# Optimization experiments

Hardware: AMD Instinct MI355X
Metric: run time of the kernel (lower is better)

Reference implementation:

```python
import jax, jax.numpy as jnp
import numpy as np

N = 100000   # nodes
E = 1000000  # edges
F_IN = 128
H = 256
G = 64       # graphs in batch
EPS = 1e-5   # BatchNorm eps


def setup_inputs() -> dict:
    key = jax.random.key(0)
    ks = jax.random.split(key, 16)
    s = 0.05
    d = {}
    d["x"] = jax.random.normal(ks[0], (N, F_IN), jnp.float32)
    d["edge_index"] = jax.random.randint(ks[1], (2, E), 0, N, dtype=jnp.int32)
    d["batch"] = jnp.sort(jax.random.randint(ks[2], (N,), 0, G, dtype=jnp.int32))
    # block1 (128 -> 256, has projection)
    d["W1"] = jax.random.normal(ks[3], (F_IN, H), jnp.float32) * s
    d["b1"] = jnp.zeros((H,), jnp.float32)
    d["g1"] = jnp.ones((H,), jnp.float32)
    d["be1"] = jnp.zeros((H,), jnp.float32)
    d["P1"] = jax.random.normal(ks[4], (F_IN, H), jnp.float32) * s
    # blocks 2-4 (256 -> 256)
    for i, k in zip((2, 3, 4), (ks[5], ks[6], ks[7])):
        d[f"W{i}"] = jax.random.normal(k, (H, H), jnp.float32) * s
        d[f"b{i}"] = jnp.zeros((H,), jnp.float32)
        d[f"g{i}"] = jnp.ones((H,), jnp.float32)
        d[f"be{i}"] = jnp.zeros((H,), jnp.float32)
    d["Wl"] = jax.random.normal(ks[8], (H, 1), jnp.float32) * s
    d["bl"] = jnp.zeros((1,), jnp.float32)
    return d


def _gcn_norm(edge_index):
    # PyG gcn_norm: add self-loops, deg from dst column, norm = d^-1/2[src]*d^-1/2[dst]
    src, dst = edge_index[0], edge_index[1]
    deg = jax.ops.segment_sum(jnp.ones((E,), jnp.float32), dst, num_segments=N) + 1.0
    dis = jax.lax.rsqrt(deg)
    enorm = dis[src] * dis[dst]          # [E] normalization per edge
    self_w = 1.0 / deg                   # self-loop weight = deg^-1
    return src, dst, enorm, self_w


def _block(x, src, dst, enorm, self_w, W, b, g, be, P=None):
    hw = x @ W                                            # [N, H]
    msg = hw[src] * enorm[:, None]                        # [E, H] gather
    agg = jax.ops.segment_sum(msg, dst, num_segments=N)   # scatter-add
    agg = agg + hw * self_w[:, None] + b                  # self-loop + bias
    # BatchNorm1d (training-mode batch statistics, biased variance)
    m = jnp.mean(agg, axis=0)
    v = jnp.var(agg, axis=0)
    out = jax.nn.relu((agg - m) * jax.lax.rsqrt(v + EPS) * g + be)
    res = x @ P if P is not None else x
    return out + res


def reference(x, edge_index, batch, W1, b1, g1, be1, P1,
              W2, b2, g2, be2, W3, b3, g3, be3, W4, b4, g4, be4, Wl, bl):
    src, dst, enorm, self_w = _gcn_norm(edge_index)
    h = _block(x, src, dst, enorm, self_w, W1, b1, g1, be1, P1)
    h = _block(h, src, dst, enorm, self_w, W2, b2, g2, be2)
    h = _block(h, src, dst, enorm, self_w, W3, b3, g3, be3)
    h = _block(h, src, dst, enorm, self_w, W4, b4, g4, be4)
    # global mean pool over graphs
    sums = jax.ops.segment_sum(h, batch, num_segments=G)                       # [G, H]
    cnt = jax.ops.segment_sum(jnp.ones((N,), jnp.float32), batch, num_segments=G)
    pooled = sums / jnp.maximum(cnt, 1.0)[:, None]
    return pooled @ Wl + bl                                                    # [G, 1]
```

## Files before the change

### kernel.cpp

```cpp
#include <hip/hip_runtime.h>
#include <cstdint>
#include <cstddef>

#define NN 100000
#define NE 1000000
#define FIN 128
#define HD 256
#define NG 64
#define BNEPS 1e-5f

typedef unsigned short ushort_t;
typedef __attribute__((ext_vector_type(8))) short bf16x8;
typedef __attribute__((ext_vector_type(4))) float f32x4;


__device__ inline float b2f(unsigned short u) {
    union { float f; unsigned int i; } x; x.i = ((unsigned int)u) << 16; return x.f;
}
__device__ inline unsigned short f2b(float f) {
    union { float f; unsigned int i; } x; x.f = f;
    unsigned int r = x.i + 0x7FFFu + ((x.i >> 16) & 1u);
    return (unsigned short)(r >> 16);
}
__device__ inline float  ld1(const unsigned short* p) { return b2f(*p); }
__device__ inline float4 ld4v(const unsigned short* p) {
    ushort4 u = *(const ushort4*)p;
    return make_float4(b2f(u.x), b2f(u.y), b2f(u.z), b2f(u.w));
}
__device__ inline float2 ld2v(const unsigned short* p) {
    ushort2 u = *(const ushort2*)p;
    return make_float2(b2f(u.x), b2f(u.y));
}
__device__ inline void st4v(unsigned short* p, float4 v) {
    ushort4 u; u.x = f2b(v.x); u.y = f2b(v.y); u.z = f2b(v.z); u.w = f2b(v.w);
    *(ushort4*)p = u;
}
__device__ inline void st2v(unsigned short* p, float2 v) {
    ushort2 u; u.x = f2b(v.x); u.y = f2b(v.y);
    *(ushort2*)p = u;
}


__global__ __launch_bounds__(256) void count_deg_k(const int* __restrict__ dst, int* __restrict__ cnt) {
    int e = blockIdx.x * 256 + threadIdx.x;
    if (e < NE) atomicAdd(&cnt[dst[e]], 1);
}

__global__ __launch_bounds__(256) void node_prep_k(const int* __restrict__ cnt,
                                                   float* __restrict__ dis, float* __restrict__ selfw) {
    int i = blockIdx.x * 256 + threadIdx.x;
    if (i < NN) {
        float d = (float)cnt[i] + 1.0f;
        dis[i] = rsqrtf(d);
        selfw[i] = 1.0f / d;
    }
}

__global__ __launch_bounds__(1024) void scan_reduce_k(const int* __restrict__ cnt, int* __restrict__ partials) {
    __shared__ int sh[1024];
    int i = blockIdx.x * 1024 + threadIdx.x;
    sh[threadIdx.x] = (i < NN) ? cnt[i] : 0;
    __syncthreads();
    for (int off = 512; off > 0; off >>= 1) {
        if (threadIdx.x < off) sh[threadIdx.x] += sh[threadIdx.x + off];
        __syncthreads();
    }
    if (threadIdx.x == 0) partials[blockIdx.x] = sh[0];
}

__global__ void scan_partials_k(int* partials, int nb) {
    if (threadIdx.x == 0 && blockIdx.x == 0) {
        int run = 0;
        for (int b = 0; b < nb; b++) { int v = partials[b]; partials[b] = run; run += v; }
    }
}

__global__ __launch_bounds__(1024) void scan_write_k(const int* __restrict__ cnt,
                                                     const int* __restrict__ partials,
                                                     int* __restrict__ rowptr) {
    __shared__ int sh[1024];
    int i = blockIdx.x * 1024 + threadIdx.x;
    int v = (i < NN) ? cnt[i] : 0;
    sh[threadIdx.x] = v;
    __syncthreads();
    for (int off = 1; off < 1024; off <<= 1) {
        int t = (threadIdx.x >= off) ? sh[threadIdx.x - off] : 0;
        __syncthreads();
        sh[threadIdx.x] += t;
        __syncthreads();
    }
    if (i < NN) rowptr[i] = partials[blockIdx.x] + sh[threadIdx.x] - v;
    if (i == NN - 1) rowptr[NN] = partials[blockIdx.x] + sh[threadIdx.x];
}

__global__ __launch_bounds__(256) void fill_csr_k(const int* __restrict__ src, const int* __restrict__ dst,
                                                  const int* __restrict__ rowptr, int* __restrict__ cursor,
                                                  const float* __restrict__ dis,
                                                  int2* __restrict__ csr) {
    int e = blockIdx.x * 256 + threadIdx.x;
    if (e < NE) {
        int d = dst[e], s = src[e];
        int pos = rowptr[d] + atomicAdd(&cursor[d], 1);
        float w = dis[s] * dis[d];
        csr[pos] = make_int2(s, __float_as_int(w));
    }
}

__global__ __launch_bounds__(256) void x2b_k(const float* __restrict__ x, unsigned short* __restrict__ xb) {
    int i = blockIdx.x * 256 + threadIdx.x;
    if (i < NN * FIN / 4) {
        float4 v = *reinterpret_cast<const float4*>(x + (size_t)i * 4);
        ushort4 u; u.x = f2b(v.x); u.y = f2b(v.y); u.z = f2b(v.z); u.w = f2b(v.w);
        *reinterpret_cast<ushort4*>(xb + (size_t)i * 4) = u;
    }
}

__global__ __launch_bounds__(256) void wt_all_k(const float* __restrict__ W1, const float* __restrict__ P1,
                                                const float* __restrict__ W2, const float* __restrict__ W3,
                                                const float* __restrict__ W4,
                                                unsigned short* __restrict__ w1t, unsigned short* __restrict__ p1t,
                                                unsigned short* __restrict__ w2t, unsigned short* __restrict__ w3t,
                                                unsigned short* __restrict__ w4t) {
    int b = blockIdx.x;
    const float* W; unsigned short* Bt; int K; int base;
    if (b < 128)      { W = W1; Bt = w1t; K = 128; base = b; }
    else if (b < 256) { W = P1; Bt = p1t; K = 128; base = b - 128; }
    else if (b < 512) { W = W2; Bt = w2t; K = 256; base = b - 256; }
    else if (b < 768) { W = W3; Bt = w3t; K = 256; base = b - 512; }
    else              { W = W4; Bt = w4t; K = 256; base = b - 768; }
    int i = base * 256 + threadIdx.x;
    if (i < K * 256) {
        int k = i >> 8, n = i & 255;
        Bt[n * K + k] = f2b(W[k * 256 + n]);
    }
}


template<int COLS>
__global__ __launch_bounds__(256) void spmm_k(const unsigned short* __restrict__ h,
                                              const int* __restrict__ rowptr,
                                              const int2* __restrict__ csr,
                                              const float* __restrict__ selfw,
                                              unsigned short* __restrict__ z) {
    const int lane = threadIdx.x & 63;
    const int row = blockIdx.x * 4 + (threadIdx.x >> 6);
    if (row >= NN) return;
    if constexpr (COLS == 256) {
        float4 a = ld4v(h + (size_t)row * COLS + lane * 4);
        float sw = selfw[row];
        float4 acc = make_float4(a.x * sw, a.y * sw, a.z * sw, a.w * sw);
        int e = rowptr[row];
        const int e1 = rowptr[row + 1];
        for (; e + 8 <= e1; e += 8) {
            int2 cc[8];
#pragma unroll
            for (int j = 0; j < 8; j++) cc[j] = csr[e + j];
            float4 hv[8];
#pragma unroll
            for (int j = 0; j < 8; j++) hv[j] = ld4v(h + (size_t)cc[j].x * COLS + lane * 4);
#pragma unroll
            for (int j = 0; j < 8; j++) {
                float w = __int_as_float(cc[j].y);
                acc.x += w * hv[j].x; acc.y += w * hv[j].y; acc.z += w * hv[j].z; acc.w += w * hv[j].w;
            }
        }
        for (; e + 4 <= e1; e += 4) {
            int2 c0 = csr[e], c1 = csr[e + 1], c2 = csr[e + 2], c3 = csr[e + 3];
            float4 h0 = ld4v(h + (size_t)c0.x * COLS + lane * 4);
            float4 h1 = ld4v(h + (size_t)c1.x * COLS + lane * 4);
            float4 h2 = ld4v(h + (size_t)c2.x * COLS + lane * 4);
            float4 h3 = ld4v(h + (size_t)c3.x * COLS + lane * 4);
            float w0 = __int_as_float(c0.y), w1 = __int_as_float(c1.y);
            float w2 = __int_as_float(c2.y), w3 = __int_as_float(c3.y);
            acc.x += w0 * h0.x; acc.y += w0 * h0.y; acc.z += w0 * h0.z; acc.w += w0 * h0.w;
            acc.x += w1 * h1.x; acc.y += w1 * h1.y; acc.z += w1 * h1.z; acc.w += w1 * h1.w;
            acc.x += w2 * h2.x; acc.y += w2 * h2.y; acc.z += w2 * h2.z; acc.w += w2 * h2.w;
            acc.x += w3 * h3.x; acc.y += w3 * h3.y; acc.z += w3 * h3.z; acc.w += w3 * h3.w;
        }
        for (; e < e1; e++) {
            int2 c = csr[e];
            float w = __int_as_float(c.y);
            float4 hv = ld4v(h + (size_t)c.x * COLS + lane * 4);
            acc.x += w * hv.x; acc.y += w * hv.y; acc.z += w * hv.z; acc.w += w * hv.w;
        }
        st4v(z + (size_t)row * COLS + lane * 4, acc);
    } else {
        float2 a = ld2v(h + (size_t)row * COLS + lane * 2);
        float sw = selfw[row];
        float2 acc = make_float2(a.x * sw, a.y * sw);
        int e = rowptr[row];
        const int e1 = rowptr[row + 1];
        for (; e + 8 <= e1; e += 8) {
            int2 cc[8];
#pragma unroll
            for (int j = 0; j < 8; j++) cc[j] = csr[e + j];
            float2 hv[8];
#pragma unroll
            for (int j = 0; j < 8; j++) hv[j] = ld2v(h + (size_t)cc[j].x * COLS + lane * 2);
#pragma unroll
            for (int j = 0; j < 8; j++) {
                float w = __int_as_float(cc[j].y);
                acc.x += w * hv[j].x; acc.y += w * hv[j].y;
            }
        }
        for (; e + 4 <= e1; e += 4) {
            int2 c0 = csr[e], c1 = csr[e + 1], c2 = csr[e + 2], c3 = csr[e + 3];
            float2 h0 = ld2v(h + (size_t)c0.x * COLS + lane * 2);
            float2 h1 = ld2v(h + (size_t)c1.x * COLS + lane * 2);
            float2 h2 = ld2v(h + (size_t)c2.x * COLS + lane * 2);
            float2 h3 = ld2v(h + (size_t)c3.x * COLS + lane * 2);
            float w0 = __int_as_float(c0.y), w1 = __int_as_float(c1.y);
            float w2 = __int_as_float(c2.y), w3 = __int_as_float(c3.y);
            acc.x += w0 * h0.x; acc.y += w0 * h0.y;
            acc.x += w1 * h1.x; acc.y += w1 * h1.y;
            acc.x += w2 * h2.x; acc.y += w2 * h2.y;
            acc.x += w3 * h3.x; acc.y += w3 * h3.y;
        }
        for (; e < e1; e++) {
            int2 c = csr[e];
            float w = __int_as_float(c.y);
            float2 hv = ld2v(h + (size_t)c.x * COLS + lane * 2);
            acc.x += w * hv.x; acc.y += w * hv.y;
        }
        st2v(z + (size_t)row * COLS + lane * 2, acc);
    }
}


#define RPB 391

template<int K, int MODE>
__global__ __launch_bounds__(512, 4) void mgemm_k(const unsigned short* __restrict__ A,
                                                  const unsigned short* __restrict__ Bt,
                                                  const float* __restrict__ bias,
                                                  unsigned short* __restrict__ C,
                                                  const float* __restrict__ scale,
                                                  const float* __restrict__ shift,
                                                  const unsigned short* __restrict__ aggin,
                                                  float* __restrict__ sums, int M) {
    constexpr int NCOLS = 128;
    constexpr int NF = NCOLS / 16;
    constexpr int SEGS = K / 8;
    constexpr int KS = K / 32;
    __shared__ char Bl[NCOLS * K * 2];
    __shared__ float sstat[2 * NCOLS];
    const int tid  = threadIdx.x;
    const int lane = tid & 63;
    const int wid  = tid >> 6;
    const int q    = lane >> 4;
    const int rl   = lane & 15;
    const int col0 = blockIdx.y * NCOLS;
    const int rbase = blockIdx.x * RPB;
    const int rend  = min(rbase + RPB, M);

    for (int s = tid; s < NCOLS * SEGS; s += 512) {
        int col = s / SEGS, j = s % SEGS;
        uint4 v = *reinterpret_cast<const uint4*>(Bt + (size_t)(col0 + col) * K + j * 8);
        *reinterpret_cast<uint4*>(Bl + col * (K * 2) + (((j) ^ (col & 7)) << 4)) = v;
    }
    if (MODE == 0 && tid < 2 * NCOLS) sstat[tid] = 0.f;
    __syncthreads();

    for (int it = 0; it < 2; it++) {
        const int row0 = rbase + it * 256 + wid * 32;
        if (row0 >= rend) continue;

        const int a0r = min(row0 + rl, M - 1);
        const int a1r = min(row0 + 16 + rl, M - 1);
        const unsigned short* pa0 = A + (size_t)a0r * K + q * 8;
        const unsigned short* pa1 = A + (size_t)a1r * K + q * 8;

        f32x4 acc[2][NF];
#pragma unroll
        for (int m = 0; m < 2; m++)
#pragma unroll
            for (int n = 0; n < NF; n++) acc[m][n] = (f32x4){0.f, 0.f, 0.f, 0.f};

#pragma unroll
        for (int ks = 0; ks < KS; ks++) {
            bf16x8 af0 = *reinterpret_cast<const bf16x8*>(pa0 + ks * 32);
            bf16x8 af1 = *reinterpret_cast<const bf16x8*>(pa1 + ks * 32);
#pragma unroll
            for (int nf = 0; nf < NF; nf++) {
                int col = nf * 16 + rl;
                bf16x8 bf = *reinterpret_cast<const bf16x8*>(Bl + col * (K * 2) + (((ks * 4 + q) ^ (col & 7)) << 4));
                acc[0][nf] = __builtin_amdgcn_mfma_f32_16x16x32_bf16(bf, af0, acc[0][nf], 0, 0, 0);
                acc[1][nf] = __builtin_amdgcn_mfma_f32_16x16x32_bf16(bf, af1, acc[1][nf], 0, 0, 0);
            }
        }

        const int g0 = row0 + rl, g1 = row0 + 16 + rl;
        const bool ok0 = g0 < rend, ok1 = g1 < rend;
#pragma unroll
        for (int nf = 0; nf < NF; nf++) {
            int cb = col0 + nf * 16 + q * 4;
            f32x4 v0 = acc[0][nf], v1 = acc[1][nf];
            if (MODE == 0) {
                float4 bb = *reinterpret_cast<const float4*>(bias + cb);
                v0[0] += bb.x; v0[1] += bb.y; v0[2] += bb.z; v0[3] += bb.w;
                v1[0] += bb.x; v1[1] += bb.y; v1[2] += bb.z; v1[3] += bb.w;
            } else {
                float4 sc = *reinterpret_cast<const float4*>(scale + cb);
                float4 sh = *reinterpret_cast<const float4*>(shift + cb);
                if (ok0) {
                    ushort4 ag = *reinterpret_cast<const ushort4*>(aggin + (size_t)g0 * HD + cb);
                    v0[0] += fmaxf(fmaf(b2f(ag.x), sc.x, sh.x), 0.f);
                    v0[1] += fmaxf(fmaf(b2f(ag.y), sc.y, sh.y), 0.f);
                    v0[2] += fmaxf(fmaf(b2f(ag.z), sc.z, sh.z), 0.f);
                    v0[3] += fmaxf(fmaf(b2f(ag.w), sc.w, sh.w), 0.f);
                }
                if (ok1) {
                    ushort4 ag = *reinterpret_cast<const ushort4*>(aggin + (size_t)g1 * HD + cb);
                    v1[0] += fmaxf(fmaf(b2f(ag.x), sc.x, sh.x), 0.f);
                    v1[1] += fmaxf(fmaf(b2f(ag.y), sc.y, sh.y), 0.f);
                    v1[2] += fmaxf(fmaf(b2f(ag.z), sc.z, sh.z), 0.f);
                    v1[3] += fmaxf(fmaf(b2f(ag.w), sc.w, sh.w), 0.f);
                }
            }
            if (ok0) {
                ushort4 u; u.x = f2b(v0[0]); u.y = f2b(v0[1]); u.z = f2b(v0[2]); u.w = f2b(v0[3]);
                *reinterpret_cast<ushort4*>(C + (size_t)g0 * HD + cb) = u;
            }
            if (ok1) {
                ushort4 u; u.x = f2b(v1[0]); u.y = f2b(v1[1]); u.z = f2b(v1[2]); u.w = f2b(v1[3]);
                *reinterpret_cast<ushort4*>(C + (size_t)g1 * HD + cb) = u;
            }
            if (MODE == 0) {
                if (!ok0) { v0[0] = v0[1] = v0[2] = v0[3] = 0.f; }
                if (!ok1) { v1[0] = v1[1] = v1[2] = v1[3] = 0.f; }
                float s[4], qq[4];
#pragma unroll
                for (int j = 0; j < 4; j++) {
                    s[j]  = v0[j] + v1[j];
                    qq[j] = v0[j] * v0[j] + v1[j] * v1[j];
                }
#pragma unroll
                for (int m = 1; m < 16; m <<= 1) {
#pragma unroll
                    for (int j = 0; j < 4; j++) {
                        s[j]  += __shfl_xor(s[j], m, 64);
                        qq[j] += __shfl_xor(qq[j], m, 64);
                    }
                }
                if (rl == 0) {
                    int cl = nf * 16 + q * 4;
#pragma unroll
                    for (int j = 0; j < 4; j++) {
                        atomicAdd(&sstat[cl + j], s[j]);
                        atomicAdd(&sstat[NCOLS + cl + j], qq[j]);
                    }
                }
            }
        }
    }

    if (MODE == 0) {
        __syncthreads();
        if (tid < NCOLS)            atomicAdd(&sums[col0 + tid], sstat[tid]);
        else if (tid < 2 * NCOLS)   atomicAdd(&sums[HD + col0 + (tid - NCOLS)], sstat[tid]);
    }
}


__global__ void bn_fin_k(const float* __restrict__ sums, const float* __restrict__ g,
                         const float* __restrict__ be, float* __restrict__ sc, float* __restrict__ sh) {
    int c = threadIdx.x;
    float m = sums[c] * (1.0f / NN);
    float v = sums[HD + c] * (1.0f / NN) - m * m;
    float s = g[c] * rsqrtf(v + BNEPS);
    sc[c] = s;
    sh[c] = be[c] - m * s;
}

__global__ __launch_bounds__(256) void epi_k(const unsigned short* __restrict__ agg,
                                             const unsigned short* __restrict__ res,
                                             const float* __restrict__ scp, const float* __restrict__ shp,
                                             unsigned short* __restrict__ out) {
    const size_t total = (size_t)NN * (HD / 4);
    size_t i = (size_t)blockIdx.x * 256 + threadIdx.x;
    const size_t stride = (size_t)gridDim.x * 256;
    for (; i < total; i += stride) {
        int cq = ((int)(i & 63)) * 4;
        float4 a = ld4v(agg + i * 4);
        float4 r = ld4v(res + i * 4);
        float4 sc = *reinterpret_cast<const float4*>(scp + cq);
        float4 sh = *reinterpret_cast<const float4*>(shp + cq);
        float4 o;
        o.x = fmaxf(fmaf(a.x, sc.x, sh.x), 0.f) + r.x;
        o.y = fmaxf(fmaf(a.y, sc.y, sh.y), 0.f) + r.y;
        o.z = fmaxf(fmaf(a.z, sc.z, sh.z), 0.f) + r.z;
        o.w = fmaxf(fmaf(a.w, sc.w, sh.w), 0.f) + r.w;
        st4v(out + i * 4, o);
    }
}


#define EP_RPB 40

__global__ __launch_bounds__(256) void epi_pool_k(const unsigned short* __restrict__ lin,
                                                  const unsigned short* __restrict__ res,
                                                  const float* __restrict__ scp, const float* __restrict__ shp,
                                                  const int* __restrict__ batch,
                                                  float* __restrict__ pooled) {
    const int c = threadIdx.x;
    const int rs = blockIdx.x * EP_RPB;
    if (rs >= NN) return;
    const int re = min(rs + EP_RPB, NN);
    const float sc = scp[c], sh = shp[c];
    float acc = 0.f;
    int cur = batch[rs];
    int r = rs;
    for (; r + 4 <= re; r += 4) {
        float a[4], rr[4]; int g[4];
#pragma unroll
        for (int j = 0; j < 4; j++) {
            a[j]  = b2f(lin[(size_t)(r + j) * HD + c]);
            rr[j] = b2f(res[(size_t)(r + j) * HD + c]);
            g[j]  = batch[r + j];
        }
#pragma unroll
        for (int j = 0; j < 4; j++) {
            if (g[j] != cur) { atomicAdd(&pooled[(size_t)cur * HD + c], acc); acc = 0.f; cur = g[j]; }
            acc += fmaxf(fmaf(a[j], sc, sh), 0.f) + rr[j];
        }
    }
    for (; r < re; r++) {
        int g = batch[r];
        if (g != cur) { atomicAdd(&pooled[(size_t)cur * HD + c], acc); acc = 0.f; cur = g; }
        float a = b2f(lin[(size_t)r * HD + c]);
        float rv = b2f(res[(size_t)r * HD + c]);
        acc += fmaxf(fmaf(a, sc, sh), 0.f) + rv;
    }
    atomicAdd(&pooled[(size_t)cur * HD + c], acc);
}

__global__ void pool_out_k(const float* __restrict__ pooled, const int* __restrict__ batch,
                           const float* __restrict__ Wl, const float* __restrict__ bl,
                           float* __restrict__ out) {
    int g = threadIdx.x;
    if (g < NG) {
        auto lb = [&](int val) {
            int lo = 0, hi = NN;
            while (lo < hi) { int mid = (lo + hi) >> 1; if (batch[mid] < val) lo = mid + 1; else hi = mid; }
            return lo;
        };
        int c0 = lb(g), c1 = lb(g + 1);
        float cn = fmaxf((float)(c1 - c0), 1.0f);
        float s = 0.f;
        for (int c = 0; c < HD; c++) s += pooled[(size_t)g * HD + c] * Wl[c];
        out[g] = s / cn + bl[0];
    }
}


static inline size_t alignup(size_t x) { return (x + 255) & ~size_t(255); }

extern "C" void kernel_launch(void* const* d_in, const int* in_sizes, int n_in,
                              void* d_out, int out_size, void* d_ws, size_t ws_size,
                              hipStream_t stream) {
    const float* x    = (const float*)d_in[0];
    const int*   ei   = (const int*)d_in[1];
    const int*   bat  = (const int*)d_in[2];
    const float* W1   = (const float*)d_in[3];
    const float* bi1  = (const float*)d_in[4];
    const float* g1   = (const float*)d_in[5];
    const float* be1  = (const float*)d_in[6];
    const float* P1   = (const float*)d_in[7];
    const float* W2   = (const float*)d_in[8];
    const float* bi2  = (const float*)d_in[9];
    const float* g2   = (const float*)d_in[10];
    const float* be2  = (const float*)d_in[11];
    const float* W3   = (const float*)d_in[12];
    const float* bi3  = (const float*)d_in[13];
    const float* g3   = (const float*)d_in[14];
    const float* be3  = (const float*)d_in[15];
    const float* W4   = (const float*)d_in[16];
    const float* bi4  = (const float*)d_in[17];
    const float* g4   = (const float*)d_in[18];
    const float* be4  = (const float*)d_in[19];
    const float* Wl   = (const float*)d_in[20];
    const float* bl   = (const float*)d_in[21];
    float* out = (float*)d_out;

    const int* e_src = ei;
    const int* e_dst = ei + NE;

    typedef unsigned short ST;
    char* p = (char*)d_ws;
    auto alloc = [&](size_t bytes) { char* q = p; p += alignup(bytes); return q; };
    ST*    fb0     = (ST*)alloc((size_t)NN * HD * sizeof(ST));
    ST*    fb1     = (ST*)alloc((size_t)NN * HD * sizeof(ST));
    ST*    fb2     = (ST*)alloc((size_t)NN * HD * sizeof(ST));
    ST*    xb      = (ST*)alloc((size_t)NN * FIN * sizeof(ST));
    float* dis     = (float*)alloc((size_t)NN * 4);
    float* selfw   = (float*)alloc((size_t)NN * 4);
    int*   rowptr  = (int*)alloc((size_t)(NN + 1) * 4);
    int2*  csr     = (int2*)alloc((size_t)NE * 8);
    int*   partials= (int*)alloc(128 * 4);
    float* bnsc    = (float*)alloc(HD * 4);
    float* bnsh    = (float*)alloc(HD * 4);
    ST*    w1t     = (ST*)alloc(256 * 128 * sizeof(ST));
    ST*    p1t     = (ST*)alloc(256 * 128 * sizeof(ST));
    ST*    w2t     = (ST*)alloc(256 * 256 * sizeof(ST));
    ST*    w3t     = (ST*)alloc(256 * 256 * sizeof(ST));
    ST*    w4t     = (ST*)alloc(256 * 256 * sizeof(ST));
    size_t zbytes = (size_t)NN * 4 + (size_t)NN * 4 + 4 * 2 * HD * 4 + (size_t)NG * HD * 4;
    char*  zbase   = alloc(zbytes);
    int*   cnt     = (int*)zbase;
    int*   cursor  = (int*)(zbase + (size_t)NN * 4);
    float* sums1   = (float*)(zbase + (size_t)NN * 8);
    float* sums2   = sums1 + 2 * HD;
    float* sums3   = sums2 + 2 * HD;
    float* sums4   = sums3 + 2 * HD;
    float* pooled  = sums4 + 2 * HD;

    const int NB = (NN + 1023) / 1024;
    dim3 gg(256, 2);

    hipMemsetAsync(zbase, 0, zbytes, stream);

    wt_all_k<<<1024, 256, 0, stream>>>(W1, P1, W2, W3, W4, w1t, p1t, w2t, w3t, w4t);
    x2b_k<<<(NN * FIN / 4 + 255) / 256, 256, 0, stream>>>(x, xb);

    count_deg_k<<<(NE + 255) / 256, 256, 0, stream>>>(e_dst, cnt);
    node_prep_k<<<(NN + 255) / 256, 256, 0, stream>>>(cnt, dis, selfw);
    scan_reduce_k<<<NB, 1024, 0, stream>>>(cnt, partials);
    scan_partials_k<<<1, 64, 0, stream>>>(partials, NB);
    scan_write_k<<<NB, 1024, 0, stream>>>(cnt, partials, rowptr);
    fill_csr_k<<<(NE + 255) / 256, 256, 0, stream>>>(e_src, e_dst, rowptr, cursor, dis, csr);

    spmm_k<128><<<NN / 4, 256, 0, stream>>>(xb, rowptr, csr, selfw, fb0);
    mgemm_k<128, 0><<<gg, 512, 0, stream>>>(fb0, w1t, bi1, fb2, nullptr, nullptr, nullptr, sums1, NN);
    bn_fin_k<<<1, 256, 0, stream>>>(sums1, g1, be1, bnsc, bnsh);
    mgemm_k<128, 1><<<gg, 512, 0, stream>>>(xb, p1t, nullptr, fb1, bnsc, bnsh, fb2, nullptr, NN);

    spmm_k<256><<<NN / 4, 256, 0, stream>>>(fb1, rowptr, csr, selfw, fb0);
    mgemm_k<256, 0><<<gg, 512, 0, stream>>>(fb0, w2t, bi2, fb2, nullptr, nullptr, nullptr, sums2, NN);
    bn_fin_k<<<1, 256, 0, stream>>>(sums2, g2, be2, bnsc, bnsh);
    epi_k<<<4096, 256, 0, stream>>>(fb2, fb1, bnsc, bnsh, fb0);

    spmm_k<256><<<NN / 4, 256, 0, stream>>>(fb0, rowptr, csr, selfw, fb1);
    mgemm_k<256, 0><<<gg, 512, 0, stream>>>(fb1, w3t, bi3, fb2, nullptr, nullptr, nullptr, sums3, NN);
    bn_fin_k<<<1, 256, 0, stream>>>(sums3, g3, be3, bnsc, bnsh);
    epi_k<<<4096, 256, 0, stream>>>(fb2, fb0, bnsc, bnsh, fb1);

    spmm_k<256><<<NN / 4, 256, 0, stream>>>(fb1, rowptr, csr, selfw, fb0);
    mgemm_k<256, 0><<<gg, 512, 0, stream>>>(fb0, w4t, bi4, fb2, nullptr, nullptr, nullptr, sums4, NN);
    bn_fin_k<<<1, 256, 0, stream>>>(sums4, g4, be4, bnsc, bnsh);
    epi_pool_k<<<(NN + EP_RPB - 1) / EP_RPB, 256, 0, stream>>>(fb2, fb1, bnsc, bnsh, bat, pooled);
    pool_out_k<<<1, 64, 0, stream>>>(pooled, bat, Wl, bl, out);
}
```

Measured before the change: 738.1 us.

## Fold BN finalize into consumers and widen GEMM blocks to all columns

Removes the separate BatchNorm finalize kernels by recomputing per-channel scale/shift from the accumulated sums inside the GEMM epilogue, epi and pool kernels. The GEMM now launches 1024-thread blocks that cover all 256 output columns, staging the full weight matrix in LDS so each A row is read once instead of twice. This trims launch count and A-operand traffic, but doubles LDS per block and forces large blocks, which may reduce occupancy and adds redundant rsqrt work per thread.

Result: slower. 757.1 us (+2.6%).

```diff
diff --git a/kernel.cpp b/kernel.cpp
--- a/kernel.cpp
+++ b/kernel.cpp
@@ -38,6 +38,13 @@
 __device__ inline void st2v(unsigned short* p, float2 v) {
     ushort2 u; u.x = f2b(v.x); u.y = f2b(v.y);
     *(ushort2*)p = u;
+}
+
+__device__ inline void bn_sc_sh(float s, float q, float g, float be, float& sc, float& sh) {
+    float m = s * (1.0f / NN);
+    float v = q * (1.0f / NN) - m * m;
+    sc = g * rsqrtf(v + BNEPS);
+    sh = be - m * sc;
 }
 
 
@@ -230,39 +237,41 @@
 #define RPB 391
 
 template<int K, int MODE>
-__global__ __launch_bounds__(512, 4) void mgemm_k(const unsigned short* __restrict__ A,
-                                                  const unsigned short* __restrict__ Bt,
-                                                  const float* __restrict__ bias,
-                                                  unsigned short* __restrict__ C,
-                                                  const float* __restrict__ scale,
-                                                  const float* __restrict__ shift,
-                                                  const unsigned short* __restrict__ aggin,
-                                                  float* __restrict__ sums, int M) {
-    constexpr int NCOLS = 128;
-    constexpr int NF = NCOLS / 16;
+__global__ __launch_bounds__(1024, 4) void mgemm_k(const unsigned short* __restrict__ A,
+                                                   const unsigned short* __restrict__ Bt,
+                                                   const float* __restrict__ bias,
+                                                   unsigned short* __restrict__ C,
+                                                   const float* __restrict__ gamma,
+                                                   const float* __restrict__ beta,
+                                                   const float* __restrict__ sums_in,
+                                                   const unsigned short* __restrict__ aggin,
+                                                   float* __restrict__ sums_out, int M) {
+    constexpr int NF = 8;
     constexpr int SEGS = K / 8;
     constexpr int KS = K / 32;
-    __shared__ char Bl[NCOLS * K * 2];
-    __shared__ float sstat[2 * NCOLS];
+    __shared__ char Bl[256 * K * 2];
+    __shared__ float sstat[512];
     const int tid  = threadIdx.x;
     const int lane = tid & 63;
     const int wid  = tid >> 6;
+    const int wr   = wid & 7;
+    const int cw   = wid >> 3;
     const int q    = lane >> 4;
     const int rl   = lane & 15;
-    const int col0 = blockIdx.y * NCOLS;
+    const int col0 = cw * 128;
     const int rbase = blockIdx.x * RPB;
     const int rend  = min(rbase + RPB, M);
 
-    for (int s = tid; s < NCOLS * SEGS; s += 512) {
+    for (int s = tid; s < 256 * SEGS; s += 1024) {
         int col = s / SEGS, j = s % SEGS;
-        uint4 v = *reinterpret_cast<const uint4*>(Bt + (size_t)(col0 + col) * K + j * 8);
-        *reinterpret_cast<uint4*>(Bl + col * (K * 2) + (((j) ^ (col & 7)) << 4)) = v;
-    }
-    if (MODE == 0 && tid < 2 * NCOLS) sstat[tid] = 0.f;
+        uint4 v = *reinterpret_cast<const uint4*>(Bt + (size_t)col * K + j * 8);
+        *reinterpret_cast<uint4*>(Bl + col * (K * 2) + ((j ^ (col & 7)) << 4)) = v;
+    }
+    if (MODE == 0 && tid < 512) sstat[tid] = 0.f;
     __syncthreads();
 
     for (int it = 0; it < 2; it++) {
-        const int row0 = rbase + it * 256 + wid * 32;
+        const int row0 = rbase + it * 256 + wr * 32;
         if (row0 >= rend) continue;
 
         const int a0r = min(row0 + rl, M - 1);
@@ -282,8 +291,8 @@
             bf16x8 af1 = *reinterpret_cast<const bf16x8*>(pa1 + ks * 32);
 #pragma unroll
             for (int nf = 0; nf < NF; nf++) {
-                int col = nf * 16 + rl;
-                bf16x8 bf = *reinterpret_cast<const bf16x8*>(Bl + col * (K * 2) + (((ks * 4 + q) ^ (col & 7)) << 4));
+                int colL = col0 + nf * 16 + rl;
+                bf16x8 bf = *reinterpret_cast<const bf16x8*>(Bl + colL * (K * 2) + (((ks * 4 + q) ^ (colL & 7)) << 4));
                 acc[0][nf] = __builtin_amdgcn_mfma_f32_16x16x32_bf16(bf, af0, acc[0][nf], 0, 0, 0);
                 acc[1][nf] = __builtin_amdgcn_mfma_f32_16x16x32_bf16(bf, af1, acc[1][nf], 0, 0, 0);
             }
@@ -300,21 +309,28 @@
                 v0[0] += bb.x; v0[1] += bb.y; v0[2] += bb.z; v0[3] += bb.w;
                 v1[0] += bb.x; v1[1] += bb.y; v1[2] += bb.z; v1[3] += bb.w;
             } else {
-                float4 sc = *reinterpret_cast<const float4*>(scale + cb);
-                float4 sh = *reinterpret_cast<const float4*>(shift + cb);
+                float4 s4 = *reinterpret_cast<const float4*>(sums_in + cb);
+                float4 q4 = *reinterpret_cast<const float4*>(sums_in + 256 + cb);
+                float4 gm = *reinterpret_cast<const float4*>(gamma + cb);
+                float4 bt = *reinterpret_cast<const float4*>(beta + cb);
+                float sc[4], sh[4];
+                bn_sc_sh(s4.x, q4.x, gm.x, bt.x, sc[0], sh[0]);
+                bn_sc_sh(s4.y, q4.y, gm.y, bt.y, sc[1], sh[1]);
+                bn_sc_sh(s4.z, q4.z, gm.z, bt.z, sc[2], sh[2]);
+                bn_sc_sh(s4.w, q4.w, gm.w, bt.w, sc[3], sh[3]);
                 if (ok0) {
                     ushort4 ag = *reinterpret_cast<const ushort4*>(aggin + (size_t)g0 * HD + cb);
-                    v0[0] += fmaxf(fmaf(b2f(ag.x), sc.x, sh.x), 0.f);
-                    v0[1] += fmaxf(fmaf(b2f(ag.y), sc.y, sh.y), 0.f);
-                    v0[2] += fmaxf(fmaf(b2f(ag.z), sc.z, sh.z), 0.f);
-                    v0[3] += fmaxf(fmaf(b2f(ag.w), sc.w, sh.w), 0.f);
+                    v0[0] += fmaxf(fmaf(b2f(ag.x), sc[0], sh[0]), 0.f);
+                    v0[1] += fmaxf(fmaf(b2f(ag.y), sc[1], sh[1]), 0.f);
+                    v0[2] += fmaxf(fmaf(b2f(ag.z), sc[2], sh[2]), 0.f);
+                    v0[3] += fmaxf(fmaf(b2f(ag.w), sc[3], sh[3]), 0.f);
                 }
                 if (ok1) {
                     ushort4 ag = *reinterpret_cast<const ushort4*>(aggin + (size_t)g1 * HD + cb);
-                    v1[0] += fmaxf(fmaf(b2f(ag.x), sc.x, sh.x), 0.f);
-                    v1[1] += fmaxf(fmaf(b2f(ag.y), sc.y, sh.y), 0.f);
-                    v1[2] += fmaxf(fmaf(b2f(ag.z), sc.z, sh.z), 0.f);
-                    v1[3] += fmaxf(fmaf(b2f(ag.w), sc.w, sh.w), 0.f);
+                    v1[0] += fmaxf(fmaf(b2f(ag.x), sc[0], sh[0]), 0.f);
+                    v1[1] += fmaxf(fmaf(b2f(ag.y), sc[1], sh[1]), 0.f);
+                    v1[2] += fmaxf(fmaf(b2f(ag.z), sc[2], sh[2]), 0.f);
+                    v1[3] += fmaxf(fmaf(b2f(ag.w), sc[3], sh[3]), 0.f);
                 }
             }
             if (ok0) {
@@ -343,11 +359,10 @@
                     }
                 }
                 if (rl == 0) {
-                    int cl = nf * 16 + q * 4;
 #pragma unroll
                     for (int j = 0; j < 4; j++) {
-                        atomicAdd(&sstat[cl + j], s[j]);
-                        atomicAdd(&sstat[NCOLS + cl + j], qq[j]);
+                        atomicAdd(&sstat[cb + j], s[j]);
+                        atomicAdd(&sstat[256 + cb + j], qq[j]);
                     }
                 }
             }
@@ -356,25 +371,16 @@
 
     if (MODE == 0) {
         __syncthreads();
-        if (tid < NCOLS)            atomicAdd(&sums[col0 + tid], sstat[tid]);
-        else if (tid < 2 * NCOLS)   atomicAdd(&sums[HD + col0 + (tid - NCOLS)], sstat[tid]);
-    }
-}
-
-
-__global__ void bn_fin_k(const float* __restrict__ sums, const float* __restrict__ g,
-                         const float* __restrict__ be, float* __restrict__ sc, float* __restrict__ sh) {
-    int c = threadIdx.x;
-    float m = sums[c] * (1.0f / NN);
-    float v = sums[HD + c] * (1.0f / NN) - m * m;
-    float s = g[c] * rsqrtf(v + BNEPS);
-    sc[c] = s;
-    sh[c] = be[c] - m * s;
-}
+        if (tid < 512) atomicAdd(&sums_out[tid], sstat[tid]);
+    }
+}
+
 
 __global__ __launch_bounds__(256) void epi_k(const unsigned short* __restrict__ agg,
                                              const unsigned short* __restrict__ res,
-                                             const float* __restrict__ scp, const float* __restrict__ shp,
+                                             const float* __restrict__ sums,
+                                             const float* __restrict__ gamma,
+                                             const float* __restrict__ beta,
                                              unsigned short* __restrict__ out) {
     const size_t total = (size_t)NN * (HD / 4);
     size_t i = (size_t)blockIdx.x * 256 + threadIdx.x;
@@ -383,13 +389,20 @@
         int cq = ((int)(i & 63)) * 4;
         float4 a = ld4v(agg + i * 4);
         float4 r = ld4v(res + i * 4);
-        float4 sc = *reinterpret_cast<const float4*>(scp + cq);
-        float4 sh = *reinterpret_cast<const float4*>(shp + cq);
+        float4 s4 = *reinterpret_cast<const float4*>(sums + cq);
+        float4 q4 = *reinterpret_cast<const float4*>(sums + 256 + cq);
+        float4 gm = *reinterpret_cast<const float4*>(gamma + cq);
+        float4 bt = *reinterpret_cast<const float4*>(beta + cq);
+        float sc0, sh0, sc1, sh1, sc2, sh2, sc3, sh3;
+        bn_sc_sh(s4.x, q4.x, gm.x, bt.x, sc0, sh0);
+        bn_sc_sh(s4.y, q4.y, gm.y, bt.y, sc1, sh1);
+        bn_sc_sh(s4.z, q4.z, gm.z, bt.z, sc2, sh2);
+        bn_sc_sh(s4.w, q4.w, gm.w, bt.w, sc3, sh3);
         float4 o;
-        o.x = fmaxf(fmaf(a.x, sc.x, sh.x), 0.f) + r.x;
-        o.y = fmaxf(fmaf(a.y, sc.y, sh.y), 0.f) + r.y;
-        o.z = fmaxf(fmaf(a.z, sc.z, sh.z), 0.f) + r.z;
-        o.w = fmaxf(fmaf(a.w, sc.w, sh.w), 0.f) + r.w;
+        o.x = fmaxf(fmaf(a.x, sc0, sh0), 0.f) + r.x;
+        o.y = fmaxf(fmaf(a.y, sc1, sh1), 0.f) + r.y;
+        o.z = fmaxf(fmaf(a.z, sc2, sh2), 0.f) + r.z;
+        o.w = fmaxf(fmaf(a.w, sc3, sh3), 0.f) + r.w;
         st4v(out + i * 4, o);
     }
 }
@@ -399,14 +412,17 @@
 
 __global__ __launch_bounds__(256) void epi_pool_k(const unsigned short* __restrict__ lin,
                                                   const unsigned short* __restrict__ res,
-                                                  const float* __restrict__ scp, const float* __restrict__ shp,
+                                                  const float* __restrict__ sums,
+                                                  const float* __restrict__ gamma,
+                                                  const float* __restrict__ beta,
                                                   const int* __restrict__ batch,
                                                   float* __restrict__ pooled) {
     const int c = threadIdx.x;
     const int rs = blockIdx.x * EP_RPB;
     if (rs >= NN) return;
     const int re = min(rs + EP_RPB, NN);
-    const float sc = scp[c], sh = shp[c];
+    float sc, sh;
+    bn_sc_sh(sums[c], sums[256 + c], gamma[c], beta[c], sc, sh);
     float acc = 0.f;
     int cur = batch[rs];
     int r = rs;
@@ -497,8 +513,6 @@
     int*   rowptr  = (int*)alloc((size_t)(NN + 1) * 4);
     int2*  csr     = (int2*)alloc((size_t)NE * 8);
     int*   partials= (int*)alloc(128 * 4);
-    float* bnsc    = (float*)alloc(HD * 4);
-    float* bnsh    = (float*)alloc(HD * 4);
     ST*    w1t     = (ST*)alloc(256 * 128 * sizeof(ST));
     ST*    p1t     = (ST*)alloc(256 * 128 * sizeof(ST));
     ST*    w2t     = (ST*)alloc(256 * 256 * sizeof(ST));
@@ -515,7 +529,6 @@
     float* pooled  = sums4 + 2 * HD;
 
     const int NB = (NN + 1023) / 1024;
-    dim3 gg(256, 2);
 
     hipMemsetAsync(zbase, 0, zbytes, stream);
 
@@ -530,23 +543,19 @@
     fill_csr_k<<<(NE + 255) / 256, 256, 0, stream>>>(e_src, e_dst, rowptr, cursor, dis, csr);
 
     spmm_k<128><<<NN / 4, 256, 0, stream>>>(xb, rowptr, csr, selfw, fb0);
-    mgemm_k<128, 0><<<gg, 512, 0, stream>>>(fb0, w1t, bi1, fb2, nullptr, nullptr, nullptr, sums1, NN);
-    bn_fin_k<<<1, 256, 0, stream>>>(sums1, g1, be1, bnsc, bnsh);
-    mgemm_k<128, 1><<<gg, 512, 0, stream>>>(xb, p1t, nullptr, fb1, bnsc, bnsh, fb2, nullptr, NN);
+    mgemm_k<128, 0><<<256, 1024, 0, stream>>>(fb0, w1t, bi1, fb2, nullptr, nullptr, nullptr, nullptr, sums1, NN);
+    mgemm_k<128, 1><<<256, 1024, 0, stream>>>(xb, p1t, nullptr, fb1, g1, be1, sums1, fb2, nullptr, NN);
 
     spmm_k<256><<<NN / 4, 256, 0, stream>>>(fb1, rowptr, csr, selfw, fb0);
-    mgemm_k<256, 0><<<gg, 512, 0, stream>>>(fb0, w2t, bi2, fb2, nullptr, nullptr, nullptr, sums2, NN);
-    bn_fin_k<<<1, 256, 0, stream>>>(sums2, g2, be2, bnsc, bnsh);
-    epi_k<<<4096, 256, 0, stream>>>(fb2, fb1, bnsc, bnsh, fb0);
+    mgemm_k<256, 0><<<256, 1024, 0, stream>>>(fb0, w2t, bi2, fb2, nullptr, nullptr, nullptr, nullptr, sums2, NN);
+    epi_k<<<4096, 256, 0, stream>>>(fb2, fb1, sums2, g2, be2, fb0);
 
     spmm_k<256><<<NN / 4, 256, 0, stream>>>(fb0, rowptr, csr, selfw, fb1);
-    mgemm_k<256, 0><<<gg, 512, 0, stream>>>(fb1, w3t, bi3, fb2, nullptr, nullptr, nullptr, sums3, NN);
-    bn_fin_k<<<1, 256, 0, stream>>>(sums3, g3, be3, bnsc, bnsh);
-    epi_k<<<4096, 256, 0, stream>>>(fb2, fb0, bnsc, bnsh, fb1);
+    mgemm_k<256, 0><<<256, 1024, 0, stream>>>(fb1, w3t, bi3, fb2, nullptr, nullptr, nullptr, nullptr, sums3, NN);
+    epi_k<<<4096, 256, 0, stream>>>(fb2, fb0, sums3, g3, be3, fb1);
 
     spmm_k<256><<<NN / 4, 256, 0, stream>>>(fb1, rowptr, csr, selfw, fb0);
-    mgemm_k<256, 0><<<gg, 512, 0, stream>>>(fb0, w4t, bi4, fb2, nullptr, nullptr, nullptr, sums4, NN);
-    bn_fin_k<<<1, 256, 0, stream>>>(sums4, g4, be4, bnsc, bnsh);
-    epi_pool_k<<<(NN + EP_RPB - 1) / EP_RPB, 256, 0, stream>>>(fb2, fb1, bnsc, bnsh, bat, pooled);
+    mgemm_k<256, 0><<<256, 1024, 0, stream>>>(fb0, w4t, bi4, fb2, nullptr, nullptr, nullptr, nullptr, sums4, NN);
+    epi_pool_k<<<(NN + EP_RPB - 1) / EP_RPB, 256, 0, stream>>>(fb2, fb1, sums4, g4, be4, bat, pooled);
     pool_out_k<<<1, 64, 0, stream>>>(pooled, bat, Wl, bl, out);
 }
```
